# Optimization experiments

Hardware: AMD Instinct MI355X
Metric: run time of the kernel (lower is better)

The kernel has to match this reference:

```python
import jax, jax.numpy as jnp
import numpy as np

N_NODES = 50000
IN_DIM = 128
OUT_DIM = 2 * IN_DIM  # GCNConv(input_dim, input_dim*2)
N_EDGES = 800000


def setup_inputs() -> dict:
    key = jax.random.key(0)
    k1, k2, k3, k4 = jax.random.split(key, 4)
    x = jax.random.normal(k1, (N_NODES, IN_DIM), dtype=jnp.float32)
    edge_index = jax.random.randint(k2, (N_EDGES, 2), 0, N_NODES, dtype=jnp.int64)
    # GCNConv linear weight [out, in] (applied as x @ W.T) and bias [out]
    scale = 1.0 / np.sqrt(IN_DIM)
    W = jax.random.normal(k3, (OUT_DIM, IN_DIM), dtype=jnp.float32) * scale
    b = jax.random.normal(k4, (OUT_DIM,), dtype=jnp.float32) * 0.01
    return {"x": x, "edge_index": edge_index, "W": W, "b": b}


def reference(x, edge_index, W, b):
    # Faithful to PyG GCNConv: add self-loops, symmetric degree normalization,
    # linear transform, scatter-sum aggregation, bias, then ReLU.
    N = x.shape[0]
    src = edge_index[:, 0]
    dst = edge_index[:, 1]
    loop = jnp.arange(N, dtype=src.dtype)
    src = jnp.concatenate([src, loop])  # [E + N]
    dst = jnp.concatenate([dst, loop])

    h = x @ W.T  # [N, OUT_DIM]

    ones = jnp.ones(dst.shape, dtype=h.dtype)
    deg = jax.ops.segment_sum(ones, dst, num_segments=N)  # in-degree incl. self-loop
    dinv = jnp.where(deg > 0, jax.lax.rsqrt(deg), 0.0)
    norm = dinv[src] * dinv[dst]  # [E + N]

    msg = h[src] * norm[:, None]  # gather + scale, [E+N, OUT_DIM]
    out = jax.ops.segment_sum(msg, dst, num_segments=N) + b  # scatter-add
    return jax.nn.relu(out)
```

## Files before the change

kernel.cpp:

```cpp
#include <hip/hip_runtime.h>

#define N_NODES 50000
#define IN_DIM  128
#define OUT_DIM 256
#define N_EDGES 800000
#define BINA_BLOCKS 128
#define EDGES_PER_BINA 6250
#define WCONV_BLOCKS 4
#define N_BUCKETS 782
#define BUCKET_CAP 1280

typedef short bf16x8 __attribute__((ext_vector_type(8)));
typedef float f32x4  __attribute__((ext_vector_type(4)));
typedef unsigned short ushort8_t __attribute__((ext_vector_type(8)));

__device__ __forceinline__ unsigned short f2bf(float f) {
    unsigned u = __float_as_uint(f);
    return (unsigned short)((u + 0x7fffu + ((u >> 16) & 1u)) >> 16);
}
__device__ __forceinline__ float bf2f(unsigned short h) {
    return __uint_as_float(((unsigned)h) << 16);
}
__device__ __forceinline__ float blo(unsigned p) { return __uint_as_float(p << 16); }
__device__ __forceinline__ float bhi(unsigned p) { return __uint_as_float(p & 0xffff0000u); }


__global__ __launch_bounds__(1024) void k_prep(const int* __restrict__ ei,
                                               int* __restrict__ bcnt,
                                               unsigned* __restrict__ bucketed,
                                               const float* __restrict__ W,
                                               unsigned short* __restrict__ Wh,
                                               unsigned short* __restrict__ Wl) {
    __shared__ int hist[N_BUCKETS];
    __shared__ int cursor[N_BUCKETS];
    int b = blockIdx.x, tid = threadIdx.x;
    if (b < BINA_BLOCKS) {
        int base = b * EDGES_PER_BINA;
        for (int t = tid; t < N_BUCKETS; t += 1024) hist[t] = 0;
        __syncthreads();
        for (int e = tid; e < EDGES_PER_BINA; e += 1024) {
            int2 p = *(const int2*)&ei[2 * (base + e)];
            atomicAdd(&hist[p.y >> 6], 1);
        }
        __syncthreads();
        for (int t = tid; t < N_BUCKETS; t += 1024) {
            int cnt = hist[t];
            cursor[t] = t * BUCKET_CAP + (cnt ? atomicAdd(&bcnt[t], cnt) : 0);
        }
        __syncthreads();
        for (int e = tid; e < EDGES_PER_BINA; e += 1024) {
            int2 p = *(const int2*)&ei[2 * (base + e)];
            int bkt = p.y >> 6;
            int pos = atomicAdd(&cursor[bkt], 1);
            if (pos < (bkt + 1) * BUCKET_CAP)
                bucketed[pos] = ((unsigned)(p.y & 63) << 16) | (unsigned)p.x;
        }
    } else {
        int t = (b - BINA_BLOCKS) * 1024 + tid;
        int base = t * 8;
        float4 a = *(const float4*)&W[base];
        float4 c = *(const float4*)&W[base + 4];
        ushort8_t h, l;
        h[0] = f2bf(a.x); h[1] = f2bf(a.y); h[2] = f2bf(a.z); h[3] = f2bf(a.w);
        h[4] = f2bf(c.x); h[5] = f2bf(c.y); h[6] = f2bf(c.z); h[7] = f2bf(c.w);
        l[0] = f2bf(a.x - bf2f(h[0])); l[1] = f2bf(a.y - bf2f(h[1]));
        l[2] = f2bf(a.z - bf2f(h[2])); l[3] = f2bf(a.w - bf2f(h[3]));
        l[4] = f2bf(c.x - bf2f(h[4])); l[5] = f2bf(c.y - bf2f(h[5]));
        l[6] = f2bf(c.z - bf2f(h[6])); l[7] = f2bf(c.w - bf2f(h[7]));
        *(ushort8_t*)&Wh[base] = h;
        *(ushort8_t*)&Wl[base] = l;
    }
}


__global__ __launch_bounds__(512) void k_degxconv(const int* __restrict__ bcnt,
                                                  const unsigned* __restrict__ bucketed,
                                                  const float* __restrict__ x,
                                                  int* __restrict__ counts,
                                                  unsigned short* __restrict__ xs) {
    __shared__ int h[64];
    __shared__ float sdinv[64];
    int b = blockIdx.x, tid = threadIdx.x;
    int node0 = b << 6;
    if (tid < 64) h[tid] = 0;
    __syncthreads();
    int ecnt = bcnt[b]; if (ecnt > BUCKET_CAP) ecnt = BUCKET_CAP;
    const unsigned* bb = bucketed + b * BUCKET_CAP;
    for (int e = tid; e < ecnt; e += 512)
        atomicAdd(&h[bb[e] >> 16], 1);
    __syncthreads();
    if (tid < 64) {
        int n = node0 + tid;
        if (n < N_NODES) counts[n] = h[tid];
        sdinv[tid] = rsqrtf((float)(h[tid] + 1));
    }
    __syncthreads();
    #pragma unroll
    for (int it = 0; it < 2; ++it) {
        int g = it * 512 + tid;
        int nl = g >> 4;
        int n = node0 + nl;
        if (n < N_NODES) {
            float d = sdinv[nl];
            int base = n * IN_DIM + (g & 15) * 8;
            float4 a = *(const float4*)&x[base];
            float4 c = *(const float4*)&x[base + 4];
            ushort8_t o;
            o[0] = f2bf(d * a.x); o[1] = f2bf(d * a.y);
            o[2] = f2bf(d * a.z); o[3] = f2bf(d * a.w);
            o[4] = f2bf(d * c.x); o[5] = f2bf(d * c.y);
            o[6] = f2bf(d * c.z); o[7] = f2bf(d * c.w);
            *(ushort8_t*)&xs[base] = o;
        }
    }
}


__global__ __launch_bounds__(512) void k_aggregate(
        const uint2* __restrict__ xs2, const int* __restrict__ counts,
        const int* __restrict__ bcnt, const unsigned* __restrict__ bucketed,
        uint2* __restrict__ yh2, uint2* __restrict__ yl2) {
    __shared__ int lsrc[BUCKET_CAP];
    __shared__ int ncnt[64], nstart[64], ncur[64];
    int b = blockIdx.x, tid = threadIdx.x;
    int node0 = b << 6;
    if (tid < 64) {
        int n = node0 + tid;
        int c = (n < N_NODES) ? counts[n] : 0;
        ncnt[tid] = c;
        int v = c;
        #pragma unroll
        for (int off = 1; off < 64; off <<= 1) {
            int u = __shfl_up(v, off);
            if (tid >= off) v += u;
        }
        nstart[tid] = v;
        ncur[tid] = v - c;
    }
    __syncthreads();
    int ecnt = bcnt[b]; if (ecnt > BUCKET_CAP) ecnt = BUCKET_CAP;
    const unsigned* bb = bucketed + b * BUCKET_CAP;
    for (int e = tid; e < ecnt; e += 512) {
        unsigned p = bb[e];
        int pos = atomicAdd(&ncur[p >> 16], 1);
        lsrc[pos] = (int)(p & 0xffffu);
    }
    __syncthreads();
    int wv = tid >> 6, lane = tid & 63;
    int hh = lane >> 5;
    int c = lane & 31;
    for (int k = 0; k < 8; ++k) {
        int ln = wv * 8 + k;
        int i = node0 + ln;
        if (i >= N_NODES) break;
        int cnt = ncnt[ln];
        float di = rsqrtf((float)(cnt + 1));
        int end = nstart[ln];
        int start = end - cnt;
        float f0 = 0.f, f1 = 0.f, f2 = 0.f, f3 = 0.f;
        if (hh == 0) {
            uint2 p = xs2[i * 32 + c];
            f0 = blo(p.x); f1 = bhi(p.x); f2 = blo(p.y); f3 = bhi(p.y);
        }
        for (int e0 = start; e0 < end; e0 += 64) {
            int ne = end - e0; if (ne > 64) ne = 64;
            int sv = (lane < ne) ? lsrc[e0 + lane] : 0;
            int pairs = ne >> 1;
            int t = 0;
            for (; t + 4 <= pairs; t += 4) {
                int s0 = __shfl(sv, 2 * t + hh);
                int s1 = __shfl(sv, 2 * t + 2 + hh);
                int s2 = __shfl(sv, 2 * t + 4 + hh);
                int s3 = __shfl(sv, 2 * t + 6 + hh);
                uint2 p0 = xs2[s0 * 32 + c];
                uint2 p1 = xs2[s1 * 32 + c];
                uint2 p2 = xs2[s2 * 32 + c];
                uint2 p3 = xs2[s3 * 32 + c];
                f0 += blo(p0.x) + blo(p1.x) + blo(p2.x) + blo(p3.x);
                f1 += bhi(p0.x) + bhi(p1.x) + bhi(p2.x) + bhi(p3.x);
                f2 += blo(p0.y) + blo(p1.y) + blo(p2.y) + blo(p3.y);
                f3 += bhi(p0.y) + bhi(p1.y) + bhi(p2.y) + bhi(p3.y);
            }
            for (; t < pairs; ++t) {
                int s = __shfl(sv, 2 * t + hh);
                uint2 p = xs2[s * 32 + c];
                f0 += blo(p.x); f1 += bhi(p.x); f2 += blo(p.y); f3 += bhi(p.y);
            }
            if (ne & 1) {
                int s = __shfl(sv, ne - 1);
                if (hh == 0) {
                    uint2 p = xs2[s * 32 + c];
                    f0 += blo(p.x); f1 += bhi(p.x); f2 += blo(p.y); f3 += bhi(p.y);
                }
            }
        }
        f0 += __shfl_xor(f0, 32);
        f1 += __shfl_xor(f1, 32);
        f2 += __shfl_xor(f2, 32);
        f3 += __shfl_xor(f3, 32);
        if (hh == 0) {
            float v0 = di * f0, v1 = di * f1, v2 = di * f2, v3 = di * f3;
            unsigned short h0 = f2bf(v0), h1 = f2bf(v1);
            unsigned short h2 = f2bf(v2), h3 = f2bf(v3);
            uint2 oh, ol;
            oh.x = (unsigned)h0 | ((unsigned)h1 << 16);
            oh.y = (unsigned)h2 | ((unsigned)h3 << 16);
            ol.x = (unsigned)f2bf(v0 - bf2f(h0)) | ((unsigned)f2bf(v1 - bf2f(h1)) << 16);
            ol.y = (unsigned)f2bf(v2 - bf2f(h2)) | ((unsigned)f2bf(v3 - bf2f(h3)) << 16);
            yh2[i * 32 + c] = oh;
            yl2[i * 32 + c] = ol;
        }
    }
}


#define LDK 136

__global__ __launch_bounds__(256) void k_gemm(
        const unsigned short* __restrict__ yh, const unsigned short* __restrict__ yl,
        const unsigned short* __restrict__ Wh, const unsigned short* __restrict__ Wl,
        const float* __restrict__ bias, float* __restrict__ out) {
    __shared__ unsigned short Ah[64 * LDK], Al[64 * LDK];
    int tid = threadIdx.x;
    int lane = tid & 63;
    int wv = tid >> 6;
    int jb = blockIdx.x * 64;
    int i0 = blockIdx.y * 64;
    int n0 = wv * 16;
    int rl = lane & 15;
    int quad = lane >> 4;

    bf16x8 bh[4], bl[4];
    #pragma unroll
    for (int ks = 0; ks < 4; ++ks) {
        int off = (jb + n0 + rl) * IN_DIM + ks * 32 + quad * 8;
        bh[ks] = *(const bf16x8*)&Wh[off];
        bl[ks] = *(const bf16x8*)&Wl[off];
    }

    #pragma unroll
    for (int it = 0; it < 4; ++it) {
        int g = it * 256 + tid;
        int r = g >> 4;
        int c8 = g & 15;
        int row = i0 + r; if (row >= N_NODES) row = N_NODES - 1;
        int ga = row * IN_DIM + c8 * 8;
        int la = r * LDK + c8 * 8;
        *(bf16x8*)&Ah[la] = *(const bf16x8*)&yh[ga];
        *(bf16x8*)&Al[la] = *(const bf16x8*)&yl[ga];
    }
    __syncthreads();

    f32x4 acc[4] = {{0.f,0.f,0.f,0.f},{0.f,0.f,0.f,0.f},{0.f,0.f,0.f,0.f},{0.f,0.f,0.f,0.f}};
    #pragma unroll
    for (int ks = 0; ks < 4; ++ks) {
        int koff = ks * 32 + quad * 8;
        #pragma unroll
        for (int mt = 0; mt < 4; ++mt) {
            bf16x8 ah = *(bf16x8*)&Ah[(mt * 16 + rl) * LDK + koff];
            bf16x8 al = *(bf16x8*)&Al[(mt * 16 + rl) * LDK + koff];
            acc[mt] = __builtin_amdgcn_mfma_f32_16x16x32_bf16(ah, bh[ks], acc[mt], 0, 0, 0);
            acc[mt] = __builtin_amdgcn_mfma_f32_16x16x32_bf16(ah, bl[ks], acc[mt], 0, 0, 0);
            acc[mt] = __builtin_amdgcn_mfma_f32_16x16x32_bf16(al, bh[ks], acc[mt], 0, 0, 0);
        }
    }

    float bv = bias[jb + n0 + rl];
    #pragma unroll
    for (int mt = 0; mt < 4; ++mt) {
        #pragma unroll
        for (int r = 0; r < 4; ++r) {
            int row = i0 + mt * 16 + quad * 4 + r;
            if (row < N_NODES) {
                float v = acc[mt][r] + bv;
                out[row * OUT_DIM + jb + n0 + rl] = fmaxf(v, 0.f);
            }
        }
    }
}


extern "C" void kernel_launch(void* const* d_in, const int* in_sizes, int n_in,
                              void* d_out, int out_size, void* d_ws, size_t ws_size,
                              hipStream_t stream) {
    const float* x  = (const float*)d_in[0];
    const int*   ei = (const int*)d_in[1];
    const float* W  = (const float*)d_in[2];
    const float* b  = (const float*)d_in[3];
    float* out = (float*)d_out;

    char* ws = (char*)d_ws;
    int*            bcnt     = (int*)(ws + 0);
    int*            counts   = (int*)(ws + 4096);
    unsigned*       bucketed = (unsigned*)(ws + 204800);
    unsigned*       yh       = (unsigned*)(ws + 4208640);
    unsigned*       yl       = (unsigned*)(ws + 17008640);
    unsigned short* xs       = (unsigned short*)(ws + 29808640);
    unsigned short* Wh       = (unsigned short*)(ws + 42608640);
    unsigned short* Wl       = (unsigned short*)(ws + 42674176);

    hipMemsetAsync(bcnt, 0, N_BUCKETS * sizeof(int), stream);

    k_prep<<<BINA_BLOCKS + WCONV_BLOCKS, 1024, 0, stream>>>(ei, bcnt, bucketed, W, Wh, Wl);
    k_degxconv<<<N_BUCKETS, 512, 0, stream>>>(bcnt, bucketed, x, counts, xs);
    k_aggregate<<<N_BUCKETS, 512, 0, stream>>>((const uint2*)xs, counts, bcnt,
                                               bucketed, (uint2*)yh, (uint2*)yl);
    dim3 g(OUT_DIM / 64, (N_NODES + 63) / 64);
    k_gemm<<<g, 256, 0, stream>>>((const unsigned short*)yh, (const unsigned short*)yl,
                                  Wh, Wl, b, out);
}
```

Before: 168.5 us.

## Fuse aggregation and GEMM into one kernel via shared-memory tile

The aggregation kernel now writes its per-node hi/lo bf16 results into a shared-memory tile and runs the split-precision MFMA GEMM against W directly, producing the final ReLU output. This removes the global round trip of the yh/yl intermediates and one kernel launch. In exchange each block now computes all 256 output columns with 8 waves, so W fragments are reloaded per block, and the extra shared memory may lower occupancy of the aggregation phase.

```diff
diff --git a/kernel.cpp b/kernel.cpp
--- a/kernel.cpp
+++ b/kernel.cpp
@@ -116,12 +116,16 @@
 }
 
 
-__global__ __launch_bounds__(512) void k_aggregate(
+#define LDK 136
+
+__global__ __launch_bounds__(512) void k_aggemm(
         const uint2* __restrict__ xs2, const int* __restrict__ counts,
         const int* __restrict__ bcnt, const unsigned* __restrict__ bucketed,
-        uint2* __restrict__ yh2, uint2* __restrict__ yl2) {
+        const unsigned short* __restrict__ Wh, const unsigned short* __restrict__ Wl,
+        const float* __restrict__ bias, float* __restrict__ out) {
     __shared__ int lsrc[BUCKET_CAP];
     __shared__ int ncnt[64], nstart[64], ncur[64];
+    __shared__ unsigned short Ah[64 * LDK], Al[64 * LDK];
     int b = blockIdx.x, tid = threadIdx.x;
     int node0 = b << 6;
     if (tid < 64) {
@@ -152,7 +156,14 @@
     for (int k = 0; k < 8; ++k) {
         int ln = wv * 8 + k;
         int i = node0 + ln;
-        if (i >= N_NODES) break;
+        if (i >= N_NODES) {
+            if (hh == 0) {
+                uint2 z; z.x = 0u; z.y = 0u;
+                *(uint2*)&Ah[ln * LDK + 4 * c] = z;
+                *(uint2*)&Al[ln * LDK + 4 * c] = z;
+            }
+            continue;
+        }
         int cnt = ncnt[ln];
         float di = rsqrtf((float)(cnt + 1));
         int end = nstart[ln];
@@ -207,73 +218,48 @@
             oh.y = (unsigned)h2 | ((unsigned)h3 << 16);
             ol.x = (unsigned)f2bf(v0 - bf2f(h0)) | ((unsigned)f2bf(v1 - bf2f(h1)) << 16);
             ol.y = (unsigned)f2bf(v2 - bf2f(h2)) | ((unsigned)f2bf(v3 - bf2f(h3)) << 16);
-            yh2[i * 32 + c] = oh;
-            yl2[i * 32 + c] = ol;
-        }
-    }
-}
-
-
-#define LDK 136
-
-__global__ __launch_bounds__(256) void k_gemm(
-        const unsigned short* __restrict__ yh, const unsigned short* __restrict__ yl,
-        const unsigned short* __restrict__ Wh, const unsigned short* __restrict__ Wl,
-        const float* __restrict__ bias, float* __restrict__ out) {
-    __shared__ unsigned short Ah[64 * LDK], Al[64 * LDK];
-    int tid = threadIdx.x;
-    int lane = tid & 63;
-    int wv = tid >> 6;
-    int jb = blockIdx.x * 64;
-    int i0 = blockIdx.y * 64;
-    int n0 = wv * 16;
+            *(uint2*)&Ah[ln * LDK + 4 * c] = oh;
+            *(uint2*)&Al[ln * LDK + 4 * c] = ol;
+        }
+    }
+    __syncthreads();
+
     int rl = lane & 15;
     int quad = lane >> 4;
-
-    bf16x8 bh[4], bl[4];
+    int n0 = wv * 32;
     #pragma unroll
-    for (int ks = 0; ks < 4; ++ks) {
-        int off = (jb + n0 + rl) * IN_DIM + ks * 32 + quad * 8;
-        bh[ks] = *(const bf16x8*)&Wh[off];
-        bl[ks] = *(const bf16x8*)&Wl[off];
-    }
-
-    #pragma unroll
-    for (int it = 0; it < 4; ++it) {
-        int g = it * 256 + tid;
-        int r = g >> 4;
-        int c8 = g & 15;
-        int row = i0 + r; if (row >= N_NODES) row = N_NODES - 1;
-        int ga = row * IN_DIM + c8 * 8;
-        int la = r * LDK + c8 * 8;
-        *(bf16x8*)&Ah[la] = *(const bf16x8*)&yh[ga];
-        *(bf16x8*)&Al[la] = *(const bf16x8*)&yl[ga];
-    }
-    __syncthreads();
-
-    f32x4 acc[4] = {{0.f,0.f,0.f,0.f},{0.f,0.f,0.f,0.f},{0.f,0.f,0.f,0.f},{0.f,0.f,0.f,0.f}};
-    #pragma unroll
-    for (int ks = 0; ks < 4; ++ks) {
-        int koff = ks * 32 + quad * 8;
+    for (int nt = 0; nt < 2; ++nt) {
+        int col = n0 + nt * 16 + rl;
+        bf16x8 bh[4], bl[4];
+        #pragma unroll
+        for (int ks = 0; ks < 4; ++ks) {
+            int off = col * IN_DIM + ks * 32 + quad * 8;
+            bh[ks] = *(const bf16x8*)&Wh[off];
+            bl[ks] = *(const bf16x8*)&Wl[off];
+        }
+        f32x4 acc[4] = {{0.f,0.f,0.f,0.f},{0.f,0.f,0.f,0.f},{0.f,0.f,0.f,0.f},{0.f,0.f,0.f,0.f}};
+        #pragma unroll
+        for (int ks = 0; ks < 4; ++ks) {
+            int koff = ks * 32 + quad * 8;
+            #pragma unroll
+            for (int mt = 0; mt < 4; ++mt) {
+                bf16x8 ah = *(bf16x8*)&Ah[(mt * 16 + rl) * LDK + koff];
+                bf16x8 al = *(bf16x8*)&Al[(mt * 16 + rl) * LDK + koff];
+                acc[mt] = __builtin_amdgcn_mfma_f32_16x16x32_bf16(ah, bh[ks], acc[mt], 0, 0, 0);
+                acc[mt] = __builtin_amdgcn_mfma_f32_16x16x32_bf16(ah, bl[ks], acc[mt], 0, 0, 0);
+                acc[mt] = __builtin_amdgcn_mfma_f32_16x16x32_bf16(al, bh[ks], acc[mt], 0, 0, 0);
+            }
+        }
+        float bv = bias[col];
         #pragma unroll
         for (int mt = 0; mt < 4; ++mt) {
-            bf16x8 ah = *(bf16x8*)&Ah[(mt * 16 + rl) * LDK + koff];
-            bf16x8 al = *(bf16x8*)&Al[(mt * 16 + rl) * LDK + koff];
-            acc[mt] = __builtin_amdgcn_mfma_f32_16x16x32_bf16(ah, bh[ks], acc[mt], 0, 0, 0);
-            acc[mt] = __builtin_amdgcn_mfma_f32_16x16x32_bf16(ah, bl[ks], acc[mt], 0, 0, 0);
-            acc[mt] = __builtin_amdgcn_mfma_f32_16x16x32_bf16(al, bh[ks], acc[mt], 0, 0, 0);
-        }
-    }
-
-    float bv = bias[jb + n0 + rl];
-    #pragma unroll
-    for (int mt = 0; mt < 4; ++mt) {
-        #pragma unroll
-        for (int r = 0; r < 4; ++r) {
-            int row = i0 + mt * 16 + quad * 4 + r;
-            if (row < N_NODES) {
-                float v = acc[mt][r] + bv;
-                out[row * OUT_DIM + jb + n0 + rl] = fmaxf(v, 0.f);
+            #pragma unroll
+            for (int r = 0; r < 4; ++r) {
+                int row = node0 + mt * 16 + quad * 4 + r;
+                if (row < N_NODES) {
+                    float v = acc[mt][r] + bv;
+                    out[row * OUT_DIM + col] = fmaxf(v, 0.f);
+                }
             }
         }
     }
@@ -293,19 +279,14 @@
     int*            bcnt     = (int*)(ws + 0);
     int*            counts   = (int*)(ws + 4096);
     unsigned*       bucketed = (unsigned*)(ws + 204800);
-    unsigned*       yh       = (unsigned*)(ws + 4208640);
-    unsigned*       yl       = (unsigned*)(ws + 17008640);
-    unsigned short* xs       = (unsigned short*)(ws + 29808640);
-    unsigned short* Wh       = (unsigned short*)(ws + 42608640);
-    unsigned short* Wl       = (unsigned short*)(ws + 42674176);
+    unsigned short* xs       = (unsigned short*)(ws + 4208640);
+    unsigned short* Wh       = (unsigned short*)(ws + 17008640);
+    unsigned short* Wl       = (unsigned short*)(ws + 17074176);
 
     hipMemsetAsync(bcnt, 0, N_BUCKETS * sizeof(int), stream);
 
     k_prep<<<BINA_BLOCKS + WCONV_BLOCKS, 1024, 0, stream>>>(ei, bcnt, bucketed, W, Wh, Wl);
     k_degxconv<<<N_BUCKETS, 512, 0, stream>>>(bcnt, bucketed, x, counts, xs);
-    k_aggregate<<<N_BUCKETS, 512, 0, stream>>>((const uint2*)xs, counts, bcnt,
-                                               bucketed, (uint2*)yh, (uint2*)yl);
-    dim3 g(OUT_DIM / 64, (N_NODES + 63) / 64);
-    k_gemm<<<g, 256, 0, stream>>>((const unsigned short*)yh, (const unsigned short*)yl,
-                                  Wh, Wl, b, out);
-}
+    k_aggemm<<<N_BUCKETS, 512, 0, stream>>>((const uint2*)xs, counts, bcnt, bucketed,
+                                            Wh, Wl, b, out);
+}
```

New measurement: 214.8 us. 1.27x slower.

## Replace global bucket atomics with per-block fixed segments in edge binning

Applied to the files above, without the earlier changes.

Edge binning now writes each (bucket, binning-block) pair into its own fixed 32-int segment, with the count stored in the first slot. This removes the separate histogram pass, the global atomic counters and the memset launch. The degree and aggregation kernels now read 128 segments per bucket, four threads per segment. The cost is a larger, sparser workspace to scan, and any edges beyond 31 per segment are silently dropped.

```diff
diff --git a/kernel.cpp b/kernel.cpp
--- a/kernel.cpp
+++ b/kernel.cpp
@@ -9,6 +9,8 @@
 #define WCONV_BLOCKS 4
 #define N_BUCKETS 782
 #define BUCKET_CAP 1280
+#define SEG_INTS 32
+#define SEG_CAP  31
 
 typedef short bf16x8 __attribute__((ext_vector_type(8)));
 typedef float f32x4  __attribute__((ext_vector_type(4)));
@@ -26,34 +28,28 @@
 
 
 __global__ __launch_bounds__(1024) void k_prep(const int* __restrict__ ei,
-                                               int* __restrict__ bcnt,
                                                unsigned* __restrict__ bucketed,
                                                const float* __restrict__ W,
                                                unsigned short* __restrict__ Wh,
                                                unsigned short* __restrict__ Wl) {
-    __shared__ int hist[N_BUCKETS];
     __shared__ int cursor[N_BUCKETS];
     int b = blockIdx.x, tid = threadIdx.x;
     if (b < BINA_BLOCKS) {
+        for (int t = tid; t < N_BUCKETS; t += 1024) cursor[t] = 1;
+        __syncthreads();
         int base = b * EDGES_PER_BINA;
-        for (int t = tid; t < N_BUCKETS; t += 1024) hist[t] = 0;
-        __syncthreads();
-        for (int e = tid; e < EDGES_PER_BINA; e += 1024) {
-            int2 p = *(const int2*)&ei[2 * (base + e)];
-            atomicAdd(&hist[p.y >> 6], 1);
-        }
-        __syncthreads();
-        for (int t = tid; t < N_BUCKETS; t += 1024) {
-            int cnt = hist[t];
-            cursor[t] = t * BUCKET_CAP + (cnt ? atomicAdd(&bcnt[t], cnt) : 0);
-        }
-        __syncthreads();
         for (int e = tid; e < EDGES_PER_BINA; e += 1024) {
             int2 p = *(const int2*)&ei[2 * (base + e)];
             int bkt = p.y >> 6;
             int pos = atomicAdd(&cursor[bkt], 1);
-            if (pos < (bkt + 1) * BUCKET_CAP)
-                bucketed[pos] = ((unsigned)(p.y & 63) << 16) | (unsigned)p.x;
+            if (pos <= SEG_CAP)
+                bucketed[(bkt * BINA_BLOCKS + b) * SEG_INTS + pos] =
+                    ((unsigned)(p.y & 63) << 16) | (unsigned)p.x;
+        }
+        __syncthreads();
+        for (int t = tid; t < N_BUCKETS; t += 1024) {
+            int cnt = cursor[t] - 1; if (cnt > SEG_CAP) cnt = SEG_CAP;
+            bucketed[(t * BINA_BLOCKS + b) * SEG_INTS] = (unsigned)cnt;
         }
     } else {
         int t = (b - BINA_BLOCKS) * 1024 + tid;
@@ -73,8 +69,7 @@
 }
 
 
-__global__ __launch_bounds__(512) void k_degxconv(const int* __restrict__ bcnt,
-                                                  const unsigned* __restrict__ bucketed,
+__global__ __launch_bounds__(512) void k_degxconv(const unsigned* __restrict__ bucketed,
                                                   const float* __restrict__ x,
                                                   int* __restrict__ counts,
                                                   unsigned short* __restrict__ xs) {
@@ -84,10 +79,14 @@
     int node0 = b << 6;
     if (tid < 64) h[tid] = 0;
     __syncthreads();
-    int ecnt = bcnt[b]; if (ecnt > BUCKET_CAP) ecnt = BUCKET_CAP;
-    const unsigned* bb = bucketed + b * BUCKET_CAP;
-    for (int e = tid; e < ecnt; e += 512)
-        atomicAdd(&h[bb[e] >> 16], 1);
+    const unsigned* bb = bucketed + b * BINA_BLOCKS * SEG_INTS;
+    {
+        int seg = tid >> 2, sub = tid & 3;
+        const unsigned* sp = bb + seg * SEG_INTS;
+        int cnt = (int)sp[0];
+        for (int j = sub; j < cnt; j += 4)
+            atomicAdd(&h[sp[1 + j] >> 16], 1);
+    }
     __syncthreads();
     if (tid < 64) {
         int n = node0 + tid;
@@ -118,7 +117,7 @@
 
 __global__ __launch_bounds__(512) void k_aggregate(
         const uint2* __restrict__ xs2, const int* __restrict__ counts,
-        const int* __restrict__ bcnt, const unsigned* __restrict__ bucketed,
+        const unsigned* __restrict__ bucketed,
         uint2* __restrict__ yh2, uint2* __restrict__ yl2) {
     __shared__ int lsrc[BUCKET_CAP];
     __shared__ int ncnt[64], nstart[64], ncur[64];
@@ -138,12 +137,16 @@
         ncur[tid] = v - c;
     }
     __syncthreads();
-    int ecnt = bcnt[b]; if (ecnt > BUCKET_CAP) ecnt = BUCKET_CAP;
-    const unsigned* bb = bucketed + b * BUCKET_CAP;
-    for (int e = tid; e < ecnt; e += 512) {
-        unsigned p = bb[e];
-        int pos = atomicAdd(&ncur[p >> 16], 1);
-        lsrc[pos] = (int)(p & 0xffffu);
+    const unsigned* bb = bucketed + b * BINA_BLOCKS * SEG_INTS;
+    {
+        int seg = tid >> 2, sub = tid & 3;
+        const unsigned* sp = bb + seg * SEG_INTS;
+        int cnt = (int)sp[0];
+        for (int j = sub; j < cnt; j += 4) {
+            unsigned p = sp[1 + j];
+            int pos = atomicAdd(&ncur[p >> 16], 1);
+            if (pos < BUCKET_CAP) lsrc[pos] = (int)(p & 0xffffu);
+        }
     }
     __syncthreads();
     int wv = tid >> 6, lane = tid & 63;
@@ -290,21 +293,18 @@
     float* out = (float*)d_out;
 
     char* ws = (char*)d_ws;
-    int*            bcnt     = (int*)(ws + 0);
-    int*            counts   = (int*)(ws + 4096);
+    int*            counts   = (int*)(ws + 0);
     unsigned*       bucketed = (unsigned*)(ws + 204800);
-    unsigned*       yh       = (unsigned*)(ws + 4208640);
-    unsigned*       yl       = (unsigned*)(ws + 17008640);
-    unsigned short* xs       = (unsigned short*)(ws + 29808640);
-    unsigned short* Wh       = (unsigned short*)(ws + 42608640);
-    unsigned short* Wl       = (unsigned short*)(ws + 42674176);
-
-    hipMemsetAsync(bcnt, 0, N_BUCKETS * sizeof(int), stream);
-
-    k_prep<<<BINA_BLOCKS + WCONV_BLOCKS, 1024, 0, stream>>>(ei, bcnt, bucketed, W, Wh, Wl);
-    k_degxconv<<<N_BUCKETS, 512, 0, stream>>>(bcnt, bucketed, x, counts, xs);
-    k_aggregate<<<N_BUCKETS, 512, 0, stream>>>((const uint2*)xs, counts, bcnt,
-                                               bucketed, (uint2*)yh, (uint2*)yl);
+    unsigned*       yh       = (unsigned*)(ws + 13017600);
+    unsigned*       yl       = (unsigned*)(ws + 25817600);
+    unsigned short* xs       = (unsigned short*)(ws + 38617600);
+    unsigned short* Wh       = (unsigned short*)(ws + 51417600);
+    unsigned short* Wl       = (unsigned short*)(ws + 51483136);
+
+    k_prep<<<BINA_BLOCKS + WCONV_BLOCKS, 1024, 0, stream>>>(ei, bucketed, W, Wh, Wl);
+    k_degxconv<<<N_BUCKETS, 512, 0, stream>>>(bucketed, x, counts, xs);
+    k_aggregate<<<N_BUCKETS, 512, 0, stream>>>((const uint2*)xs, counts, bucketed,
+                                               (uint2*)yh, (uint2*)yl);
     dim3 g(OUT_DIM / 64, (N_NODES + 63) / 64);
     k_gemm<<<g, 256, 0, stream>>>((const unsigned short*)yh, (const unsigned short*)yl,
                                   Wh, Wl, b, out);
```

New measurement: 169.6 us. No clear change (+0.6%).
